# Kernel optimization log

Hardware: AMD Instinct MI355X
Metric: run time of the kernel (lower is better)

Reference implementation:

```python
import jax, jax.numpy as jnp
import numpy as np
from jax import lax

B, T, C = 4, 2048, 2048
H, S = 32, 64
HEAD_SIZE_DIVISOR = 8.0
LN_EPS = 1e-5


def setup_inputs() -> dict:
    key = jax.random.key(0)
    ks = jax.random.split(key, 12)
    scale = 0.02
    return {
        "hidden": jax.random.normal(ks[0], (B, T, C), jnp.float32),
        "state_kv": jnp.zeros((B, H, S, S), jnp.float32),
        "time_decay": jax.random.normal(ks[1], (H, S), jnp.float32) * 0.5,
        "time_faaaa": jax.random.normal(ks[2], (H, S), jnp.float32) * 0.5,
        "time_mix_key": jax.random.uniform(ks[3], (1, 1, C), jnp.float32),
        "time_mix_value": jax.random.uniform(ks[4], (1, 1, C), jnp.float32),
        "time_mix_receptance": jax.random.uniform(ks[5], (1, 1, C), jnp.float32),
        "time_mix_gate": jax.random.uniform(ks[6], (1, 1, C), jnp.float32),
        "key_w": jax.random.normal(ks[7], (C, C), jnp.float32) * scale,
        "value_w": jax.random.normal(ks[8], (C, C), jnp.float32) * scale,
        "receptance_w": jax.random.normal(ks[9], (C, C), jnp.float32) * scale,
        "gate_w": jax.random.normal(ks[10], (C, C), jnp.float32) * scale,
        "output_w": jax.random.normal(ks[11], (C, C), jnp.float32) * scale,
        "ln_w": jnp.ones((C,), jnp.float32),
        "ln_b": jnp.zeros((C,), jnp.float32),
    }


def _rwkv5_scan(r, k, v, w, u, state0):
    # r,k,v: [B,T,H,S]; w,u: [H,S]; state0: [B,H,S,S]
    w_ = w[None, :, :, None]  # decay broadcast over value dim
    u_ = u[None, :, :, None]  # time_first (bonus) broadcast over value dim

    def step(state, rkv):
        rt, kt, vt = rkv  # each [B,H,S]
        a = kt[:, :, :, None] * vt[:, :, None, :]      # outer product [B,H,S,S]
        o = jnp.einsum("bhs,bhsd->bhd", rt, u_ * a + state)
        state = a + w_ * state
        return state, o

    rt = jnp.moveaxis(r, 1, 0)  # [T,B,H,S]
    kt = jnp.moveaxis(k, 1, 0)
    vt = jnp.moveaxis(v, 1, 0)
    state_f, out = lax.scan(step, state0, (rt, kt, vt))
    return jnp.moveaxis(out, 0, 1), state_f  # [B,T,H,S], [B,H,S,S]


def reference(hidden, state_kv, time_decay, time_faaaa, time_mix_key,
              time_mix_value, time_mix_receptance, time_mix_gate,
              key_w, value_w, receptance_w, gate_w, output_w, ln_w, ln_b):
    B_, T_, C_ = hidden.shape
    H_, S_ = time_faaaa.shape

    # time shift: prepend zero row, drop last (state=None path)
    shifted = jnp.pad(hidden, ((0, 0), (1, 0), (0, 0)))[:, :-1]

    mix = lambda m: hidden * m + shifted * (1.0 - m)
    k = mix(time_mix_key) @ key_w.T
    v = mix(time_mix_value) @ value_w.T
    r = mix(time_mix_receptance) @ receptance_w.T
    gate = jax.nn.silu(mix(time_mix_gate) @ gate_w.T)

    r = r.reshape(B_, T_, H_, S_)
    k = k.reshape(B_, T_, H_, S_)
    v = v.reshape(B_, T_, H_, S_)

    w = jnp.exp(-jnp.exp(time_decay))  # [H,S]
    out, state_f = _rwkv5_scan(r, k, v, w, time_faaaa, state_kv)

    # GroupNorm over H groups of size S, applied per (b,t) row
    x = out.reshape(B_ * T_, H_, S_) / HEAD_SIZE_DIVISOR
    mu = jnp.mean(x, axis=-1, keepdims=True)
    var = jnp.var(x, axis=-1, keepdims=True)
    xn = (x - mu) * lax.rsqrt(var + LN_EPS)
    xn = xn.reshape(B_ * T_, H_ * S_) * ln_w + ln_b

    out = xn.reshape(B_, T_, C_) * gate
    out = out @ output_w.T
    return out, state_f
```

## Files before the change

### kernel.cpp

```cpp
#include <hip/hip_runtime.h>
#include <hip/hip_bf16.h>

typedef unsigned short u16;
typedef __bf16 bf16x8 __attribute__((ext_vector_type(8)));
typedef unsigned short ushort8v __attribute__((ext_vector_type(8)));
typedef float f32x4 __attribute__((ext_vector_type(4)));
typedef float f32x8 __attribute__((ext_vector_type(8)));

#define B_ 4
#define T_ 2048
#define C_ 2048
#define H_ 32
#define S_ 64

__device__ __forceinline__ u16 f2bf(float x) {
  unsigned int u = __float_as_uint(x);
  unsigned int r = (u + 0x7fffu + ((u >> 16) & 1u)) >> 16;
  return (u16)r;
}
__device__ __forceinline__ float bf2f(u16 x) {
  return __uint_as_float(((unsigned int)x) << 16);
}
__device__ __forceinline__ void gload_lds16(const void* g, void* l) {
  __builtin_amdgcn_global_load_lds(
      (const __attribute__((address_space(1))) void*)g,
      (__attribute__((address_space(3))) void*)l, 16, 0, 0);
}

#define VM10 asm volatile("s_waitcnt vmcnt(10)" ::: "memory")
#define VM8 asm volatile("s_waitcnt vmcnt(8)" ::: "memory")
#define VM0 asm volatile("s_waitcnt vmcnt(0)" ::: "memory")
#define LGKM0 asm volatile("s_waitcnt lgkmcnt(0)" ::: "memory")
#define BARR __builtin_amdgcn_s_barrier()
#define SCB __builtin_amdgcn_sched_barrier(0)

__global__ __launch_bounds__(256) void mix_cast_kernel(
    const float* __restrict__ hidden, const float* __restrict__ mixp,
    u16* __restrict__ out) {
  int idx = blockIdx.x * 256 + threadIdx.x;
  int c4 = idx & 511;
  int bt = idx >> 9;
  int t = bt & (T_ - 1);
  float4 h = reinterpret_cast<const float4*>(hidden)[idx];
  float4 m = reinterpret_cast<const float4*>(mixp)[c4];
  float4 sh = make_float4(0.f, 0.f, 0.f, 0.f);
  if (t != 0) sh = reinterpret_cast<const float4*>(hidden)[idx - 512];
  ushort4 o;
  o.x = f2bf(h.x * m.x + sh.x * (1.f - m.x));
  o.y = f2bf(h.y * m.y + sh.y * (1.f - m.y));
  o.z = f2bf(h.z * m.z + sh.z * (1.f - m.z));
  o.w = f2bf(h.w * m.w + sh.w * (1.f - m.w));
  reinterpret_cast<ushort4*>(out)[idx] = o;
}

__global__ __launch_bounds__(256) void mix4_cast_kernel(
    const float* __restrict__ hidden,
    const float* __restrict__ mK, const float* __restrict__ mV,
    const float* __restrict__ mR, const float* __restrict__ mG,
    u16* __restrict__ oK, u16* __restrict__ oV,
    u16* __restrict__ oR, u16* __restrict__ oG) {
  int idx = blockIdx.x * 256 + threadIdx.x;
  int c4 = idx & 511;
  int bt = idx >> 9;
  int t = bt & (T_ - 1);
  float4 h = reinterpret_cast<const float4*>(hidden)[idx];
  float4 sh = make_float4(0.f, 0.f, 0.f, 0.f);
  if (t != 0) sh = reinterpret_cast<const float4*>(hidden)[idx - 512];
  float4 m;
  ushort4 o;
#define DOMIX(MP, OP)                                          \
  m = reinterpret_cast<const float4*>(MP)[c4];                 \
  o.x = f2bf(h.x * m.x + sh.x * (1.f - m.x));                  \
  o.y = f2bf(h.y * m.y + sh.y * (1.f - m.y));                  \
  o.z = f2bf(h.z * m.z + sh.z * (1.f - m.z));                  \
  o.w = f2bf(h.w * m.w + sh.w * (1.f - m.w));                  \
  reinterpret_cast<ushort4*>(OP)[idx] = o;
  DOMIX(mK, oK)
  DOMIX(mV, oV)
  DOMIX(mR, oR)
  DOMIX(mG, oG)
#undef DOMIX
}

__global__ __launch_bounds__(256) void conv_bf16_kernel(
    const float* __restrict__ in, u16* __restrict__ out, int n4) {
  int i = blockIdx.x * 256 + threadIdx.x;
  if (i >= n4) return;
  float4 v = reinterpret_cast<const float4*>(in)[i];
  ushort4 o;
  o.x = f2bf(v.x); o.y = f2bf(v.y); o.z = f2bf(v.z); o.w = f2bf(v.w);
  reinterpret_cast<ushort4*>(out)[i] = o;
}

__global__ __launch_bounds__(256) void conv4_bf16_kernel(
    const float* __restrict__ w0, const float* __restrict__ w1,
    const float* __restrict__ w2, const float* __restrict__ w3,
    u16* __restrict__ o0, u16* __restrict__ o1,
    u16* __restrict__ o2, u16* __restrict__ o3) {
  int wsel = blockIdx.x >> 12;
  int i = (blockIdx.x & 4095) * 256 + threadIdx.x;
  const float* in = (wsel == 0) ? w0 : (wsel == 1) ? w1 : (wsel == 2) ? w2 : w3;
  u16* out = (wsel == 0) ? o0 : (wsel == 1) ? o1 : (wsel == 2) ? o2 : o3;
  float4 v = reinterpret_cast<const float4*>(in)[i];
  ushort4 o;
  o.x = f2bf(v.x); o.y = f2bf(v.y); o.z = f2bf(v.z); o.w = f2bf(v.w);
  reinterpret_cast<ushort4*>(out)[i] = o;
}

template <typename OT>
__global__ __launch_bounds__(512, 2) void gemm_bt256(
    const u16* __restrict__ A, const u16* __restrict__ Bm,
    OT* __restrict__ C, int M, int N, int K) {
  __shared__ u16 Asl[4][8192];
  __shared__ u16 Bsl[4][8192];
  const int tid = threadIdx.x, lane = tid & 63, w = tid >> 6;
  const int wr = w >> 2, wc = w & 3;
  const int a15 = lane & 15, g4 = lane >> 4;
  const int nbn = N >> 8;
  const int nwg = gridDim.x, bid = blockIdx.x, cpx = nwg >> 3;
  const int swz = (bid & 7) * cpx + (bid >> 3);
  const int bm = swz / nbn, bn = swz % nbn;
  const int Ar0 = bm * 256, Br0 = bn * 256;

  const int rowoff = w * 32 + (lane >> 2);
  const int colswz = ((lane & 3) ^ ((lane >> 3) & 3)) * 8;
  const u16* Agl = A + (size_t)(Ar0 + rowoff) * K + colswz;
  const u16* Bgl = Bm + (size_t)(Br0 + rowoff) * K + colswz;
  const int lb = w * 1024;

  const int rdc = (((lane >> 4) ^ ((lane >> 1) & 3))) * 8;
  const int arow = wr * 128 + a15;
  const int brow = wc * 64 + a15;

  f32x4 acc[8][4];
#pragma unroll
  for (int m = 0; m < 8; m++)
#pragma unroll
    for (int n = 0; n < 4; n++) acc[m][n] = (f32x4){0.f, 0.f, 0.f, 0.f};

  auto STA = [&](int ktile, int kk, int slot) {
    const u16* g = Agl + ktile * 64 + kk * 32;
    gload_lds16(g, &Asl[slot][lb]);
    gload_lds16(g + (size_t)16 * K, &Asl[slot][lb + 512]);
  };
  auto STB = [&](int ktile, int kk, int slot) {
    const u16* g = Bgl + ktile * 64 + kk * 32;
    gload_lds16(g, &Bsl[slot][lb]);
    gload_lds16(g + (size_t)16 * K, &Bsl[slot][lb + 512]);
  };
  auto LOADF = [&](int P, int kk, bf16x8 (&af)[8], bf16x8 (&bv)[4]) {
    const u16* As_ = Asl[P * 2 + kk];
    const u16* Bs_ = Bsl[P * 2 + kk];
#pragma unroll
    for (int mf = 0; mf < 8; mf++)
      af[mf] = __builtin_bit_cast(
          bf16x8, *reinterpret_cast<const ushort8v*>(&As_[(arow + mf * 16) * 32 + rdc]));
#pragma unroll
    for (int nf = 0; nf < 4; nf++)
      bv[nf] = __builtin_bit_cast(
          bf16x8, *reinterpret_cast<const ushort8v*>(&Bs_[(brow + nf * 16) * 32 + rdc]));
  };
  auto MM = [&](bf16x8 (&af)[8], bf16x8 (&bv)[4]) {
    __builtin_amdgcn_s_setprio(1);
#pragma unroll
    for (int mf = 0; mf < 8; mf++)
#pragma unroll
      for (int nf = 0; nf < 4; nf++)
        acc[mf][nf] =
            __builtin_amdgcn_mfma_f32_16x16x32_bf16(af[mf], bv[nf], acc[mf][nf], 0, 0, 0);
    __builtin_amdgcn_s_setprio(0);
  };

  bf16x8 f0A[8], f1A[8];
  bf16x8 f0B[4], f1B[4];

  const int NT = K >> 6;
  STA(0, 0, 0); STB(0, 0, 0);
  STA(0, 1, 1); STB(0, 1, 1);
  STA(1, 0, 2); STB(1, 0, 2);
  VM8;
  BARR;
  LOADF(0, 0, f0A, f0B);

  for (int T = 0; T + 2 < NT; ++T) {
    int P = T & 1, Q = P ^ 1;
    STA(T + 1, 1, Q * 2 + 1); STB(T + 1, 1, Q * 2 + 1);
    VM10; BARR; SCB;
    LOADF(P, 1, f1A, f1B);
    MM(f0A, f0B);
    BARR;
    STA(T + 2, 0, P * 2 + 0); STB(T + 2, 0, P * 2 + 0);
    VM10; BARR; SCB;
    LOADF(Q, 0, f0A, f0B);
    MM(f1A, f1B);
    BARR;
  }
  {
    int T = NT - 2, P = T & 1, Q = P ^ 1;
    STA(T + 1, 1, Q * 2 + 1); STB(T + 1, 1, Q * 2 + 1);
    VM10; BARR; SCB;
    LOADF(P, 1, f1A, f1B);
    MM(f0A, f0B);
    BARR;
    VM8; BARR; SCB;
    LOADF(Q, 0, f0A, f0B);
    MM(f1A, f1B);
    BARR;
  }
  {
    int P = (NT - 1) & 1;
    VM0; BARR; SCB;
    LOADF(P, 1, f1A, f1B);
    MM(f0A, f0B);
    LGKM0;
    BARR;
    MM(f1A, f1B);
  }

  if constexpr (sizeof(OT) == 2) {
    u16* ep = (w < 4) ? Asl[w] : Bsl[w - 4];
#pragma unroll
    for (int mfg = 0; mfg < 8; mfg++)
#pragma unroll
      for (int q = 0; q < 4; q++)
#pragma unroll
        for (int nf = 0; nf < 4; nf++)
          ep[(mfg * 16 + g4 * 4 + q) * 64 + nf * 16 + a15] = f2bf(acc[mfg][nf][q]);
    OT* cbase = C + (size_t)(Ar0 + wr * 128) * N + Br0 + wc * 64;
#pragma unroll
    for (int i = 0; i < 16; i++) {
      int id = lane + 64 * i;
      int row = id >> 3, k16 = id & 7;
      ushort8v v8 = *reinterpret_cast<const ushort8v*>(&ep[row * 64 + k16 * 8]);
      *reinterpret_cast<ushort8v*>(cbase + (size_t)row * N + k16 * 8) = v8;
    }
  } else {
    int crow0 = Ar0 + wr * 128 + g4 * 4;
    int ccol0 = Br0 + wc * 64 + a15;
#pragma unroll
    for (int mfg = 0; mfg < 8; mfg++) {
#pragma unroll
      for (int q = 0; q < 4; q++) {
        OT* cp = C + (size_t)(crow0 + mfg * 16 + q) * N + ccol0;
#pragma unroll
        for (int nf = 0; nf < 4; nf++) cp[nf * 16] = (OT)acc[mfg][nf][q];
      }
    }
  }
}

template <int CHL>
__global__ __launch_bounds__(64) void scan_phase1_mfma(
    const u16* __restrict__ Kb, const u16* __restrict__ Vb,
    const float* __restrict__ td, float* __restrict__ chunks) {
  constexpr int NCH = T_ / CHL;
  constexpr int LDW = CHL + 8;
  __shared__ u16 Ash[64 * LDW];
  __shared__ u16 Vsh[64 * LDW];
  int lane = threadIdx.x & 63;
  int gw = blockIdx.x;
  int c = gw & (NCH - 1), bh = gw / NCH;
  int h = bh & 31, b = bh >> 5;

  size_t base = ((size_t)b * T_ + (size_t)c * CHL) * C_ + h * 64 + lane;
  const u16* Kp = Kb + base;
  const u16* Vp = Vb + base;

  {
    float w = __expf(-__expf(td[h * 64 + lane]));
    u16* Arow = &Ash[lane * LDW];
    float p = 1.f;
#pragma unroll
    for (int i4 = CHL - 4; i4 >= 0; i4 -= 4) {
      float a3 = bf2f(Kp[(size_t)(i4 + 3) * C_]) * p; p *= w;
      float a2 = bf2f(Kp[(size_t)(i4 + 2) * C_]) * p; p *= w;
      float a1 = bf2f(Kp[(size_t)(i4 + 1) * C_]) * p; p *= w;
      float a0 = bf2f(Kp[(size_t)(i4 + 0) * C_]) * p; p *= w;
      ushort4 pk;
      pk.x = f2bf(a0); pk.y = f2bf(a1); pk.z = f2bf(a2); pk.w = f2bf(a3);
      *reinterpret_cast<ushort4*>(&Arow[i4]) = pk;
    }
  }
  {
    u16* Vrow = &Vsh[lane * LDW];
#pragma unroll
    for (int i4 = 0; i4 < CHL; i4 += 4) {
      ushort4 pk;
      pk.x = Vp[(size_t)(i4 + 0) * C_];
      pk.y = Vp[(size_t)(i4 + 1) * C_];
      pk.z = Vp[(size_t)(i4 + 2) * C_];
      pk.w = Vp[(size_t)(i4 + 3) * C_];
      *reinterpret_cast<ushort4*>(&Vrow[i4]) = pk;
    }
  }

  f32x4 acc[4][4];
#pragma unroll
  for (int m = 0; m < 4; m++)
#pragma unroll
    for (int n = 0; n < 4; n++) acc[m][n] = (f32x4){0.f, 0.f, 0.f, 0.f};

#pragma unroll
  for (int kb = 0; kb < CHL / 32; kb++) {
    int ko = kb * 32 + (lane >> 4) * 8;
    bf16x8 Af[4], Bf[4];
#pragma unroll
    for (int m = 0; m < 4; m++) {
      ushort8v t8 = *reinterpret_cast<const ushort8v*>(&Ash[(m * 16 + (lane & 15)) * LDW + ko]);
      Af[m] = __builtin_bit_cast(bf16x8, t8);
    }
#pragma unroll
    for (int n = 0; n < 4; n++) {
      ushort8v t8 = *reinterpret_cast<const ushort8v*>(&Vsh[(n * 16 + (lane & 15)) * LDW + ko]);
      Bf[n] = __builtin_bit_cast(bf16x8, t8);
    }
#pragma unroll
    for (int m = 0; m < 4; m++)
#pragma unroll
      for (int n = 0; n < 4; n++)
        acc[m][n] = __builtin_amdgcn_mfma_f32_16x16x32_bf16(Af[m], Bf[n], acc[m][n], 0, 0, 0);
  }

  float* outp = chunks + (((size_t)c * B_ + b) * H_ + h) * 4096;
  int r0 = (lane >> 4) * 4, c0 = lane & 15;
#pragma unroll
  for (int m = 0; m < 4; m++)
#pragma unroll
    for (int n = 0; n < 4; n++)
#pragma unroll
      for (int q = 0; q < 4; q++)
        outp[(size_t)(m * 16 + r0 + q) * 64 + n * 16 + c0] = acc[m][n][q];
}

template <int NCH, int CHL>
__global__ __launch_bounds__(256) void scan_phase1(
    const u16* __restrict__ Kb, const u16* __restrict__ Vb,
    const float* __restrict__ td, float* __restrict__ chunks) {
  int lane = threadIdx.x & 63;
  int gw = (blockIdx.x * 256 + threadIdx.x) >> 6;
  int c = gw & (NCH - 1), bh = gw / NCH;
  int h = bh & 31, b = bh >> 5;
  const float* tdh = td + h * 64;
  float wreg[64];
#pragma unroll
  for (int s = 0; s < 64; s++) wreg[s] = __expf(-__expf(tdh[s]));
  float st[64];
#pragma unroll
  for (int s = 0; s < 64; s++) st[s] = 0.f;
  size_t base = ((size_t)b * T_ + (size_t)c * CHL) * C_ + h * 64 + lane;
  const u16* Kp = Kb + base;
  const u16* Vp = Vb + base;
  for (int t = 0; t < CHL; t++) {
    float kcur = bf2f(Kp[(size_t)t * C_]), vcur = bf2f(Vp[(size_t)t * C_]);
#pragma unroll
    for (int s = 0; s < 64; s++) {
      float ks = __shfl(kcur, s);
      st[s] = fmaf(wreg[s], st[s], ks * vcur);
    }
  }
  float* outp = chunks + (((size_t)c * B_ + b) * H_ + h) * 4096 + lane;
#pragma unroll
  for (int s = 0; s < 64; s++) outp[s * 64] = st[s];
}

template <int NCH, int CHL>
__global__ __launch_bounds__(256) void scan_phase2(
    const float* __restrict__ st0, const float* __restrict__ td,
    float* __restrict__ chunks, float* __restrict__ state_out) {
  int idx = blockIdx.x * 256 + threadIdx.x;
  int h = (idx >> 12) & 31;
  int s = (idx >> 6) & 63;
  float wL = __expf(-(float)CHL * __expf(td[h * 64 + s]));
  float st = st0[idx];
#pragma unroll
  for (int cc = 0; cc < NCH; cc++) {
    size_t off = (size_t)cc * 524288 + idx;
    float sc = chunks[off];
    chunks[off] = st;
    st = fmaf(wL, st, sc);
  }
  state_out[idx] = st;
}

__global__ __launch_bounds__(256) void scan_phase3_mfma(
    const u16* __restrict__ Rb, const u16* __restrict__ Kb,
    const u16* __restrict__ Vb, const float* __restrict__ td,
    const float* __restrict__ tf, const float* __restrict__ chunks,
    const u16* __restrict__ Gb, const float* __restrict__ lnw,
    const float* __restrict__ lnb, u16* __restrict__ Y) {
  __shared__ __align__(16) u16 smem[4][5248];
  int lane = threadIdx.x & 63, wib = threadIdx.x >> 6;
  int gw = blockIdx.x * 4 + wib;
  int c = gw & 31, bh = gw >> 5;
  int h = bh & 31, b = bh >> 5;
  int a = lane & 15, g = lane >> 4;
  int h0 = h * 64;

  u16* Kt = smem[wib];
  u16* Vt = Kt + 1024;
  u16* StT = Vt + 1024;
  u16* AT = StT + 2560;

  f32x8 sA[2], sB[2], sC[2];
#pragma unroll
  for (int kk = 0; kk < 2; kk++) {
#pragma unroll
    for (int e = 0; e < 8; e++) {
      int s = kk * 32 + g * 8 + e;
      float ew = __expf(td[h0 + s]);
      sA[kk][e] = __expf(-(float)a * ew);
      sB[kk][e] = __expf(-((float)a - 8.f) * ew);
      sC[kk][e] = __expf(-(7.f - (float)a) * ew);
    }
  }
  f32x4 sE[4];
  f32x4 ewD;
#pragma unroll
  for (int ms = 0; ms < 4; ms++) {
    ewD[ms] = __expf(td[h0 + ms * 16 + a]);
#pragma unroll
    for (int q = 0; q < 4; q++)
      sE[ms][q] = __expf(-16.f * __expf(td[h0 + ms * 16 + g * 4 + q]));
  }

  f32x4 St[4][4];
  const float* cpc = chunks + (((size_t)c * B_ + b) * H_ + h) * 4096;
#pragma unroll
  for (int ms = 0; ms < 4; ms++)
#pragma unroll
    for (int nd = 0; nd < 4; nd++)
#pragma unroll
      for (int q = 0; q < 4; q++)
        St[ms][nd][q] = cpc[(size_t)(ms * 16 + g * 4 + q) * 64 + nd * 16 + a];

#pragma unroll
  for (int z = 0; z < 6; z++) {
    int idx = z * 64 + lane;
    int row = idx / 24, col = 16 + idx % 24;
    AT[row * 40 + col] = 0;
  }

  size_t tbase = ((size_t)b * T_ + (size_t)c * 64) * C_ + h0;

  for (int sb = 0; sb < 4; sb++) {
    size_t rb0 = tbase + (size_t)(sb * 16) * C_;

    ushort8v r8[2], k8[2];
#pragma unroll
    for (int kk = 0; kk < 2; kk++) {
      r8[kk] = *reinterpret_cast<const ushort8v*>(Rb + rb0 + (size_t)a * C_ + kk * 32 + g * 8);
      k8[kk] = *reinterpret_cast<const ushort8v*>(Kb + rb0 + (size_t)a * C_ + kk * 32 + g * 8);
    }
    {
      int srow = lane >> 3;
      int scol = (lane & 7) * 8;
      *reinterpret_cast<ushort8v*>(&Kt[srow * 64 + scol]) =
          *reinterpret_cast<const ushort8v*>(Kb + rb0 + (size_t)srow * C_ + scol);
      *reinterpret_cast<ushort8v*>(&Kt[(srow + 8) * 64 + scol]) =
          *reinterpret_cast<const ushort8v*>(Kb + rb0 + (size_t)(srow + 8) * C_ + scol);
      *reinterpret_cast<ushort8v*>(&Vt[srow * 64 + scol]) =
          *reinterpret_cast<const ushort8v*>(Vb + rb0 + (size_t)srow * C_ + scol);
      *reinterpret_cast<ushort8v*>(&Vt[(srow + 8) * 64 + scol]) =
          *reinterpret_cast<const ushort8v*>(Vb + rb0 + (size_t)(srow + 8) * C_ + scol);
    }

    f32x4 O[4];
#pragma unroll
    for (int nd = 0; nd < 4; nd++) O[nd] = (f32x4){0.f, 0.f, 0.f, 0.f};

#pragma unroll
    for (int kk = 0; kk < 2; kk++) {
#pragma unroll
      for (int msl = 0; msl < 2; msl++) {
        int ms = kk * 2 + msl;
#pragma unroll
        for (int nd = 0; nd < 4; nd++) {
          ushort4 pk;
          pk.x = f2bf(St[ms][nd][0]); pk.y = f2bf(St[ms][nd][1]);
          pk.z = f2bf(St[ms][nd][2]); pk.w = f2bf(St[ms][nd][3]);
          *reinterpret_cast<ushort4*>(&StT[(a + nd * 16) * 40 + msl * 16 + g * 4]) = pk;
        }
      }
      ushort8v rt;
#pragma unroll
      for (int e = 0; e < 8; e++) rt[e] = f2bf(bf2f(r8[kk][e]) * sA[kk][e]);
      bf16x8 rtf = __builtin_bit_cast(bf16x8, rt);
#pragma unroll
      for (int nd = 0; nd < 4; nd++) {
        ushort8v sfr = *reinterpret_cast<const ushort8v*>(&StT[(a + nd * 16) * 40 + g * 8]);
        O[nd] = __builtin_amdgcn_mfma_f32_16x16x32_bf16(
            rtf, __builtin_bit_cast(bf16x8, sfr), O[nd], 0, 0, 0);
      }
    }

    float p = 0.f;
    {
      uintptr_t ta = (uintptr_t)(tf + h0);
      asm volatile("" : "+v"(ta));
      const float* tfp = (const float*)ta;
#pragma unroll
      for (int kk = 0; kk < 2; kk++) {
        float4 t0 = *reinterpret_cast<const float4*>(tfp + kk * 32 + g * 8);
        float4 t1 = *reinterpret_cast<const float4*>(tfp + kk * 32 + g * 8 + 4);
        float tv[8] = {t0.x, t0.y, t0.z, t0.w, t1.x, t1.y, t1.z, t1.w};
#pragma unroll
        for (int e = 0; e < 8; e++)
          p = fmaf(bf2f(r8[kk][e]) * tv[e], bf2f(k8[kk][e]), p);
      }
    }
    p += __shfl_xor(p, 16);
    p += __shfl_xor(p, 32);

    f32x4 Am = (f32x4){0.f, 0.f, 0.f, 0.f};
#pragma unroll
    for (int kk = 0; kk < 2; kk++) {
      ushort8v kh, rh;
#pragma unroll
      for (int e = 0; e < 8; e++) {
        kh[e] = f2bf(bf2f(k8[kk][e]) * sC[kk][e]);
        rh[e] = f2bf(bf2f(r8[kk][e]) * sB[kk][e]);
      }
      Am = __builtin_amdgcn_mfma_f32_16x16x32_bf16(
          __builtin_bit_cast(bf16x8, kh), __builtin_bit_cast(bf16x8, rh), Am, 0, 0, 0);
    }
    {
      ushort4 aw;
#pragma unroll
      for (int q = 0; q < 4; q++) {
        int jr = g * 4 + q;
        float v = (jr < a) ? Am[q] : ((jr == a) ? p : 0.f);
        ((u16*)&aw)[q] = f2bf(v);
      }
      *reinterpret_cast<ushort4*>(&AT[a * 40 + g * 4]) = aw;
    }
    bf16x8 afrag;
    {
      ushort8v t8 = *reinterpret_cast<const ushort8v*>(&AT[a * 40 + g * 8]);
      afrag = __builtin_bit_cast(bf16x8, t8);
    }

    bf16x8 vfrag[4];
#pragma unroll
    for (int nd = 0; nd < 4; nd++) {
      ushort8v t8;
      if (g < 2) {
#pragma unroll
        for (int e = 0; e < 8; e++) t8[e] = Vt[(g * 8 + e) * 64 + a + nd * 16];
      } else {
#pragma unroll
        for (int e = 0; e < 8; e++) t8[e] = 0;
      }
      vfrag[nd] = __builtin_bit_cast(bf16x8, t8);
    }

#pragma unroll
    for (int nd = 0; nd < 4; nd++)
      O[nd] = __builtin_amdgcn_mfma_f32_16x16x32_bf16(afrag, vfrag[nd], O[nd], 0, 0, 0);

#pragma unroll
    for (int ms = 0; ms < 4; ms++)
#pragma unroll
      for (int nd = 0; nd < 4; nd++)
#pragma unroll
        for (int q = 0; q < 4; q++) St[ms][nd][q] *= sE[ms][q];

#pragma unroll
    for (int ms = 0; ms < 4; ms++) {
      ushort8v kt8;
      if (g < 2) {
#pragma unroll
        for (int e = 0; e < 8; e++) {
          int j = g * 8 + e;
          float f = bf2f(Kt[j * 64 + ms * 16 + a]) * __expf(-(15.f - (float)j) * ewD[ms]);
          kt8[e] = f2bf(f);
        }
      } else {
#pragma unroll
        for (int e = 0; e < 8; e++) kt8[e] = 0;
      }
      bf16x8 kf = __builtin_bit_cast(bf16x8, kt8);
#pragma unroll
      for (int nd = 0; nd < 4; nd++)
        St[ms][nd] = __builtin_amdgcn_mfma_f32_16x16x32_bf16(kf, vfrag[nd], St[ms][nd], 0, 0, 0);
    }

#pragma unroll
    for (int nd = 0; nd < 4; nd++)
#pragma unroll
      for (int q = 0; q < 4; q++) O[nd][q] *= 0.125f;
    {
      uintptr_t la = (uintptr_t)(lnw + h0);
      uintptr_t lba = (uintptr_t)(lnb + h0);
      asm volatile("" : "+v"(la), "+v"(lba));
      const float* lwp = (const float*)la;
      const float* lbp = (const float*)lba;
#pragma unroll
      for (int q = 0; q < 4; q++) {
        float ssum = O[0][q] + O[1][q] + O[2][q] + O[3][q];
        ssum += __shfl_xor(ssum, 1); ssum += __shfl_xor(ssum, 2);
        ssum += __shfl_xor(ssum, 4); ssum += __shfl_xor(ssum, 8);
        float mean = ssum * (1.f / 64.f);
        float vv = 0.f;
#pragma unroll
        for (int nd = 0; nd < 4; nd++) {
          float d = O[nd][q] - mean;
          vv = fmaf(d, d, vv);
        }
        vv += __shfl_xor(vv, 1); vv += __shfl_xor(vv, 2);
        vv += __shfl_xor(vv, 4); vv += __shfl_xor(vv, 8);
        float rs = rsqrtf(vv * (1.f / 64.f) + 1e-5f);
        size_t rowoff = rb0 + (size_t)(g * 4 + q) * C_;
#pragma unroll
        for (int nd = 0; nd < 4; nd++) {
          float xn = (O[nd][q] - mean) * rs;
          float gv = bf2f(Gb[rowoff + nd * 16 + a]);
          float sg = gv / (1.f + __expf(-gv));
          Y[rowoff + nd * 16 + a] = f2bf((xn * lwp[nd * 16 + a] + lbp[nd * 16 + a]) * sg);
        }
      }
    }
  }
}

template <int NCH, int CHL>
__global__ __launch_bounds__(256) void scan_phase3(
    const u16* __restrict__ Rb, const u16* __restrict__ Kb,
    const u16* __restrict__ Vb, const float* __restrict__ td,
    const float* __restrict__ tf, const float* __restrict__ chunks,
    const u16* __restrict__ Gb, const float* __restrict__ lnw,
    const float* __restrict__ lnb, u16* __restrict__ Y) {
  int lane = threadIdx.x & 63;
  int gw = (blockIdx.x * 256 + threadIdx.x) >> 6;
  int c = gw & (NCH - 1), bh = gw / NCH;
  int h = bh & 31, b = bh >> 5;
  const float* tdh = td + h * 64;
  float wreg[64];
#pragma unroll
  for (int s = 0; s < 64; s++) wreg[s] = __expf(-__expf(tdh[s]));
  float u_own = tf[h * 64 + lane];
  float lw = lnw[h * 64 + lane];
  float lb = lnb[h * 64 + lane];
  float st[64];
  const float* cp = chunks + (((size_t)c * B_ + b) * H_ + h) * 4096 + lane;
#pragma unroll
  for (int s = 0; s < 64; s++) st[s] = cp[s * 64];
  size_t base = ((size_t)b * T_ + (size_t)c * CHL) * C_ + h * 64 + lane;
  const u16* Rp = Rb + base;
  const u16* Kp = Kb + base;
  const u16* Vp = Vb + base;
  const u16* Gp = Gb + base;
  u16* Yp = Y + base;
  for (int t = 0; t < CHL; t++) {
    float rcur = bf2f(Rp[(size_t)t * C_]);
    float kcur = bf2f(Kp[(size_t)t * C_]);
    float vcur = bf2f(Vp[(size_t)t * C_]);
    float p = rcur * u_own * kcur;
#pragma unroll
    for (int off = 32; off >= 1; off >>= 1) p += __shfl_xor(p, off);
    float acc = 0.f;
#pragma unroll
    for (int s = 0; s < 64; s++) {
      float rs = __shfl(rcur, s);
      float ks = __shfl(kcur, s);
      acc = fmaf(rs, st[s], acc);
      st[s] = fmaf(wreg[s], st[s], ks * vcur);
    }
    float o = fmaf(p, vcur, acc);
    float x = o * 0.125f;
    float sum = x;
#pragma unroll
    for (int off = 32; off >= 1; off >>= 1) sum += __shfl_xor(sum, off);
    float mean = sum * (1.f / 64.f);
    float d = x - mean;
    float v2 = d * d;
#pragma unroll
    for (int off = 32; off >= 1; off >>= 1) v2 += __shfl_xor(v2, off);
    float var = v2 * (1.f / 64.f);
    float xn = d * rsqrtf(var + 1e-5f);
    float gg = bf2f(Gp[(size_t)t * C_]);
    float sg = gg / (1.f + __expf(-gg));
    Yp[(size_t)t * C_] = f2bf((xn * lw + lb) * sg);
  }
}

extern "C" void kernel_launch(void* const* d_in, const int* in_sizes, int n_in,
                              void* d_out, int out_size, void* d_ws, size_t ws_size,
                              hipStream_t stream) {
  const float* hidden = (const float*)d_in[0];
  const float* state0 = (const float*)d_in[1];
  const float* td = (const float*)d_in[2];
  const float* tf = (const float*)d_in[3];
  const float* mk = (const float*)d_in[4];
  const float* mv = (const float*)d_in[5];
  const float* mr = (const float*)d_in[6];
  const float* mg = (const float*)d_in[7];
  const float* kw = (const float*)d_in[8];
  const float* vw = (const float*)d_in[9];
  const float* rw = (const float*)d_in[10];
  const float* gw = (const float*)d_in[11];
  const float* ow = (const float*)d_in[12];
  const float* lnw = (const float*)d_in[13];
  const float* lnb = (const float*)d_in[14];

  float* out = (float*)d_out;
  float* state_f = out + (size_t)B_ * T_ * C_;

  const size_t MBe = (size_t)B_ * T_ * C_;
  const size_t chunks32 = (size_t)32 * B_ * H_ * S_ * S_ * 4;

  size_t bigNeed = 4 * MBe * 2 + (size_t)C_ * C_ * 2 + 4 * MBe * 2 + chunks32;
  bool useBig = (ws_size >= bigNeed);

  dim3 blk(256);
  int mixGrid = (B_ * T_ * C_ / 4) / 256;
  int convN4 = C_ * C_ / 4;
  int convGrid = convN4 / 256;
  int gemmGrid = (B_ * T_ / 256) * (C_ / 256);
  dim3 gblk(512);

  if (useBig) {
    char* ws = (char*)d_ws;
    u16* mixR = (u16*)ws;  ws += MBe * 2;
    u16* mixK = (u16*)ws;  ws += MBe * 2;
    u16* mixV = (u16*)ws;  ws += MBe * 2;
    u16* mixG = (u16*)ws;  ws += MBe * 2;
    u16* wb = (u16*)ws;    ws += (size_t)C_ * C_ * 2;
    u16* rb = (u16*)ws;    ws += MBe * 2;
    u16* kb = (u16*)ws;    ws += MBe * 2;
    u16* vb = (u16*)ws;    ws += MBe * 2;
    u16* gb = (u16*)ws;    ws += MBe * 2;
    float* chunks = (float*)ws;
    u16* wbK = (u16*)chunks;
    u16* wbV = wbK + (size_t)C_ * C_;
    u16* wbG = wbV + (size_t)C_ * C_;

    mix4_cast_kernel<<<mixGrid, blk, 0, stream>>>(hidden, mk, mv, mr, mg,
                                                  mixK, mixV, mixR, mixG);
    conv4_bf16_kernel<<<4 * convGrid, blk, 0, stream>>>(rw, kw, vw, gw,
                                                        wb, wbK, wbV, wbG);
    gemm_bt256<u16><<<gemmGrid, gblk, 0, stream>>>(mixR, wb, rb, B_ * T_, C_, C_);
    gemm_bt256<u16><<<gemmGrid, gblk, 0, stream>>>(mixK, wbK, kb, B_ * T_, C_, C_);
    gemm_bt256<u16><<<gemmGrid, gblk, 0, stream>>>(mixV, wbV, vb, B_ * T_, C_, C_);
    gemm_bt256<u16><<<gemmGrid, gblk, 0, stream>>>(mixG, wbG, gb, B_ * T_, C_, C_);

    scan_phase1_mfma<64><<<B_ * H_ * 32, dim3(64), 0, stream>>>(kb, vb, td, chunks);
    scan_phase2<32, 64><<<2048, blk, 0, stream>>>(state0, td, chunks, state_f);
    scan_phase3_mfma<<<(B_ * H_ * 32) / 4, blk, 0, stream>>>(rb, kb, vb, td, tf, chunks, gb, lnw, lnb, mixR);

    conv_bf16_kernel<<<convGrid, blk, 0, stream>>>(ow, wb, convN4);
    gemm_bt256<float><<<gemmGrid, gblk, 0, stream>>>(mixR, wb, out, B_ * T_, C_, C_);
    return;
  }

  char* ws = (char*)d_ws;
  u16* mixA = (u16*)ws;    ws += MBe * 2;
  u16* wb = (u16*)ws;      ws += (size_t)C_ * C_ * 2;
  u16* rb = (u16*)ws;      ws += MBe * 2;
  u16* kb = (u16*)ws;      ws += MBe * 2;
  u16* vb = (u16*)ws;      ws += MBe * 2;
  u16* gb = (u16*)ws;      ws += MBe * 2;
  float* chunks = (float*)ws;
  size_t fixed = (size_t)(ws - (char*)d_ws);
  bool use32 = (ws_size >= fixed + chunks32);

  mix_cast_kernel<<<mixGrid, blk, 0, stream>>>(hidden, mr, mixA);
  conv_bf16_kernel<<<convGrid, blk, 0, stream>>>(rw, wb, convN4);
  gemm_bt256<u16><<<gemmGrid, gblk, 0, stream>>>(mixA, wb, rb, B_ * T_, C_, C_);
  mix_cast_kernel<<<mixGrid, blk, 0, stream>>>(hidden, mk, mixA);
  conv_bf16_kernel<<<convGrid, blk, 0, stream>>>(kw, wb, convN4);
  gemm_bt256<u16><<<gemmGrid, gblk, 0, stream>>>(mixA, wb, kb, B_ * T_, C_, C_);
  mix_cast_kernel<<<mixGrid, blk, 0, stream>>>(hidden, mv, mixA);
  conv_bf16_kernel<<<convGrid, blk, 0, stream>>>(vw, wb, convN4);
  gemm_bt256<u16><<<gemmGrid, gblk, 0, stream>>>(mixA, wb, vb, B_ * T_, C_, C_);
  mix_cast_kernel<<<mixGrid, blk, 0, stream>>>(hidden, mg, mixA);
  conv_bf16_kernel<<<convGrid, blk, 0, stream>>>(gw, wb, convN4);
  gemm_bt256<u16><<<gemmGrid, gblk, 0, stream>>>(mixA, wb, gb, B_ * T_, C_, C_);

  if (use32) {
    scan_phase1_mfma<64><<<B_ * H_ * 32, dim3(64), 0, stream>>>(kb, vb, td, chunks);
    scan_phase2<32, 64><<<2048, blk, 0, stream>>>(state0, td, chunks, state_f);
    scan_phase3_mfma<<<(B_ * H_ * 32) / 4, blk, 0, stream>>>(rb, kb, vb, td, tf, chunks, gb, lnw, lnb, mixA);
  } else {
    scan_phase1<16, 128><<<(B_ * H_ * 16) / 4, blk, 0, stream>>>(kb, vb, td, chunks);
    scan_phase2<16, 128><<<2048, blk, 0, stream>>>(state0, td, chunks, state_f);
    scan_phase3<16, 128><<<(B_ * H_ * 16) / 4, blk, 0, stream>>>(rb, kb, vb, td, tf, chunks, gb, lnw, lnb, mixA);
  }

  conv_bf16_kernel<<<convGrid, blk, 0, stream>>>(ow, wb, convN4);
  gemm_bt256<float><<<gemmGrid, gblk, 0, stream>>>(mixA, wb, out, B_ * T_, C_, C_);
}
```

Measured before the change: 690.1 us.

## Split scan phase3 value dimension across two waves per chunk with shared GroupNorm stats

The chunked scan output kernel now assigns two waves to each (batch, head, chunk) unit, each owning half of the value columns. This halves per-wave state registers and MFMA work and doubles the number of waves. GroupNorm statistics become a single-pass sum and sum-of-squares, exchanged between the paired waves through shared memory with a block barrier every subblock. Each wave still redundantly loads K/V/R and builds the intra-chunk attention matrix. The one-pass variance is less numerically robust than the previous two-pass form.

```diff
diff --git a/kernel.cpp b/kernel.cpp
--- a/kernel.cpp
+++ b/kernel.cpp
@@ -382,15 +382,17 @@
   state_out[idx] = st;
 }
 
-__global__ __launch_bounds__(256) void scan_phase3_mfma(
+__global__ __launch_bounds__(256) void scan_phase3_mfma2(
     const u16* __restrict__ Rb, const u16* __restrict__ Kb,
     const u16* __restrict__ Vb, const float* __restrict__ td,
     const float* __restrict__ tf, const float* __restrict__ chunks,
     const u16* __restrict__ Gb, const float* __restrict__ lnw,
     const float* __restrict__ lnb, u16* __restrict__ Y) {
-  __shared__ __align__(16) u16 smem[4][5248];
+  __shared__ __align__(16) u16 smem[4][4096];
+  __shared__ float gnscr[2][2][2][4][4][2];
   int lane = threadIdx.x & 63, wib = threadIdx.x >> 6;
-  int gw = blockIdx.x * 4 + wib;
+  int unit = wib >> 1, wiu = wib & 1;
+  int gw = blockIdx.x * 2 + unit;
   int c = gw & 31, bh = gw >> 5;
   int h = bh & 31, b = bh >> 5;
   int a = lane & 15, g = lane >> 4;
@@ -399,9 +401,9 @@
   u16* Kt = smem[wib];
   u16* Vt = Kt + 1024;
   u16* StT = Vt + 1024;
-  u16* AT = StT + 2560;
-
-  f32x8 sA[2], sB[2], sC[2];
+  u16* AT = StT + 1280;
+
+  f32x8 sA[2], sB[2], sC[2], uA[2];
 #pragma unroll
   for (int kk = 0; kk < 2; kk++) {
 #pragma unroll
@@ -411,6 +413,7 @@
       sA[kk][e] = __expf(-(float)a * ew);
       sB[kk][e] = __expf(-((float)a - 8.f) * ew);
       sC[kk][e] = __expf(-(7.f - (float)a) * ew);
+      uA[kk][e] = tf[h0 + s];
     }
   }
   f32x4 sE[4];
@@ -422,16 +425,23 @@
     for (int q = 0; q < 4; q++)
       sE[ms][q] = __expf(-16.f * __expf(td[h0 + ms * 16 + g * 4 + q]));
   }
-
-  f32x4 St[4][4];
+  float lwv[2], lbv[2];
+#pragma unroll
+  for (int ndl = 0; ndl < 2; ndl++) {
+    int nd_g = wiu * 2 + ndl;
+    lwv[ndl] = lnw[h0 + nd_g * 16 + a];
+    lbv[ndl] = lnb[h0 + nd_g * 16 + a];
+  }
+
+  f32x4 St[4][2];
   const float* cpc = chunks + (((size_t)c * B_ + b) * H_ + h) * 4096;
 #pragma unroll
   for (int ms = 0; ms < 4; ms++)
 #pragma unroll
-    for (int nd = 0; nd < 4; nd++)
+    for (int ndl = 0; ndl < 2; ndl++)
 #pragma unroll
       for (int q = 0; q < 4; q++)
-        St[ms][nd][q] = cpc[(size_t)(ms * 16 + g * 4 + q) * 64 + nd * 16 + a];
+        St[ms][ndl][q] = cpc[(size_t)(ms * 16 + g * 4 + q) * 64 + (wiu * 2 + ndl) * 16 + a];
 
 #pragma unroll
   for (int z = 0; z < 6; z++) {
@@ -464,9 +474,9 @@
           *reinterpret_cast<const ushort8v*>(Vb + rb0 + (size_t)(srow + 8) * C_ + scol);
     }
 
-    f32x4 O[4];
-#pragma unroll
-    for (int nd = 0; nd < 4; nd++) O[nd] = (f32x4){0.f, 0.f, 0.f, 0.f};
+    f32x4 O[2];
+#pragma unroll
+    for (int ndl = 0; ndl < 2; ndl++) O[ndl] = (f32x4){0.f, 0.f, 0.f, 0.f};
 
 #pragma unroll
     for (int kk = 0; kk < 2; kk++) {
@@ -474,11 +484,11 @@
       for (int msl = 0; msl < 2; msl++) {
         int ms = kk * 2 + msl;
 #pragma unroll
-        for (int nd = 0; nd < 4; nd++) {
+        for (int ndl = 0; ndl < 2; ndl++) {
           ushort4 pk;
-          pk.x = f2bf(St[ms][nd][0]); pk.y = f2bf(St[ms][nd][1]);
-          pk.z = f2bf(St[ms][nd][2]); pk.w = f2bf(St[ms][nd][3]);
-          *reinterpret_cast<ushort4*>(&StT[(a + nd * 16) * 40 + msl * 16 + g * 4]) = pk;
+          pk.x = f2bf(St[ms][ndl][0]); pk.y = f2bf(St[ms][ndl][1]);
+          pk.z = f2bf(St[ms][ndl][2]); pk.w = f2bf(St[ms][ndl][3]);
+          *reinterpret_cast<ushort4*>(&StT[(a + ndl * 16) * 40 + msl * 16 + g * 4]) = pk;
         }
       }
       ushort8v rt;
@@ -486,28 +496,19 @@
       for (int e = 0; e < 8; e++) rt[e] = f2bf(bf2f(r8[kk][e]) * sA[kk][e]);
       bf16x8 rtf = __builtin_bit_cast(bf16x8, rt);
 #pragma unroll
-      for (int nd = 0; nd < 4; nd++) {
-        ushort8v sfr = *reinterpret_cast<const ushort8v*>(&StT[(a + nd * 16) * 40 + g * 8]);
-        O[nd] = __builtin_amdgcn_mfma_f32_16x16x32_bf16(
-            rtf, __builtin_bit_cast(bf16x8, sfr), O[nd], 0, 0, 0);
+      for (int ndl = 0; ndl < 2; ndl++) {
+        ushort8v sfr = *reinterpret_cast<const ushort8v*>(&StT[(a + ndl * 16) * 40 + g * 8]);
+        O[ndl] = __builtin_amdgcn_mfma_f32_16x16x32_bf16(
+            rtf, __builtin_bit_cast(bf16x8, sfr), O[ndl], 0, 0, 0);
       }
     }
 
     float p = 0.f;
-    {
-      uintptr_t ta = (uintptr_t)(tf + h0);
-      asm volatile("" : "+v"(ta));
-      const float* tfp = (const float*)ta;
-#pragma unroll
-      for (int kk = 0; kk < 2; kk++) {
-        float4 t0 = *reinterpret_cast<const float4*>(tfp + kk * 32 + g * 8);
-        float4 t1 = *reinterpret_cast<const float4*>(tfp + kk * 32 + g * 8 + 4);
-        float tv[8] = {t0.x, t0.y, t0.z, t0.w, t1.x, t1.y, t1.z, t1.w};
-#pragma unroll
-        for (int e = 0; e < 8; e++)
-          p = fmaf(bf2f(r8[kk][e]) * tv[e], bf2f(k8[kk][e]), p);
-      }
-    }
+#pragma unroll
+    for (int kk = 0; kk < 2; kk++)
+#pragma unroll
+      for (int e = 0; e < 8; e++)
+        p = fmaf(bf2f(r8[kk][e]) * uA[kk][e], bf2f(k8[kk][e]), p);
     p += __shfl_xor(p, 16);
     p += __shfl_xor(p, 32);
 
@@ -539,30 +540,31 @@
       afrag = __builtin_bit_cast(bf16x8, t8);
     }
 
-    bf16x8 vfrag[4];
-#pragma unroll
-    for (int nd = 0; nd < 4; nd++) {
+    bf16x8 vfrag[2];
+#pragma unroll
+    for (int ndl = 0; ndl < 2; ndl++) {
+      int nd_g = wiu * 2 + ndl;
       ushort8v t8;
       if (g < 2) {
 #pragma unroll
-        for (int e = 0; e < 8; e++) t8[e] = Vt[(g * 8 + e) * 64 + a + nd * 16];
+        for (int e = 0; e < 8; e++) t8[e] = Vt[(g * 8 + e) * 64 + a + nd_g * 16];
       } else {
 #pragma unroll
         for (int e = 0; e < 8; e++) t8[e] = 0;
       }
-      vfrag[nd] = __builtin_bit_cast(bf16x8, t8);
-    }
-
-#pragma unroll
-    for (int nd = 0; nd < 4; nd++)
-      O[nd] = __builtin_amdgcn_mfma_f32_16x16x32_bf16(afrag, vfrag[nd], O[nd], 0, 0, 0);
+      vfrag[ndl] = __builtin_bit_cast(bf16x8, t8);
+    }
+
+#pragma unroll
+    for (int ndl = 0; ndl < 2; ndl++)
+      O[ndl] = __builtin_amdgcn_mfma_f32_16x16x32_bf16(afrag, vfrag[ndl], O[ndl], 0, 0, 0);
 
 #pragma unroll
     for (int ms = 0; ms < 4; ms++)
 #pragma unroll
-      for (int nd = 0; nd < 4; nd++)
-#pragma unroll
-        for (int q = 0; q < 4; q++) St[ms][nd][q] *= sE[ms][q];
+      for (int ndl = 0; ndl < 2; ndl++)
+#pragma unroll
+        for (int q = 0; q < 4; q++) St[ms][ndl][q] *= sE[ms][q];
 
 #pragma unroll
     for (int ms = 0; ms < 4; ms++) {
@@ -580,43 +582,48 @@
       }
       bf16x8 kf = __builtin_bit_cast(bf16x8, kt8);
 #pragma unroll
-      for (int nd = 0; nd < 4; nd++)
-        St[ms][nd] = __builtin_amdgcn_mfma_f32_16x16x32_bf16(kf, vfrag[nd], St[ms][nd], 0, 0, 0);
-    }
-
-#pragma unroll
-    for (int nd = 0; nd < 4; nd++)
-#pragma unroll
-      for (int q = 0; q < 4; q++) O[nd][q] *= 0.125f;
-    {
-      uintptr_t la = (uintptr_t)(lnw + h0);
-      uintptr_t lba = (uintptr_t)(lnb + h0);
-      asm volatile("" : "+v"(la), "+v"(lba));
-      const float* lwp = (const float*)la;
-      const float* lbp = (const float*)lba;
+      for (int ndl = 0; ndl < 2; ndl++)
+        St[ms][ndl] = __builtin_amdgcn_mfma_f32_16x16x32_bf16(kf, vfrag[ndl], St[ms][ndl], 0, 0, 0);
+    }
+
+#pragma unroll
+    for (int ndl = 0; ndl < 2; ndl++)
+#pragma unroll
+      for (int q = 0; q < 4; q++) O[ndl][q] *= 0.125f;
+    float ps[4], pq[4];
+#pragma unroll
+    for (int q = 0; q < 4; q++) {
+      float s2 = O[0][q] + O[1][q];
+      float q2 = O[0][q] * O[0][q] + O[1][q] * O[1][q];
+      s2 += __shfl_xor(s2, 1); q2 += __shfl_xor(q2, 1);
+      s2 += __shfl_xor(s2, 2); q2 += __shfl_xor(q2, 2);
+      s2 += __shfl_xor(s2, 4); q2 += __shfl_xor(q2, 4);
+      s2 += __shfl_xor(s2, 8); q2 += __shfl_xor(q2, 8);
+      ps[q] = s2; pq[q] = q2;
+    }
+    if (a == 0) {
 #pragma unroll
       for (int q = 0; q < 4; q++) {
-        float ssum = O[0][q] + O[1][q] + O[2][q] + O[3][q];
-        ssum += __shfl_xor(ssum, 1); ssum += __shfl_xor(ssum, 2);
-        ssum += __shfl_xor(ssum, 4); ssum += __shfl_xor(ssum, 8);
-        float mean = ssum * (1.f / 64.f);
-        float vv = 0.f;
-#pragma unroll
-        for (int nd = 0; nd < 4; nd++) {
-          float d = O[nd][q] - mean;
-          vv = fmaf(d, d, vv);
-        }
-        vv += __shfl_xor(vv, 1); vv += __shfl_xor(vv, 2);
-        vv += __shfl_xor(vv, 4); vv += __shfl_xor(vv, 8);
-        float rs = rsqrtf(vv * (1.f / 64.f) + 1e-5f);
-        size_t rowoff = rb0 + (size_t)(g * 4 + q) * C_;
-#pragma unroll
-        for (int nd = 0; nd < 4; nd++) {
-          float xn = (O[nd][q] - mean) * rs;
-          float gv = bf2f(Gb[rowoff + nd * 16 + a]);
-          float sg = gv / (1.f + __expf(-gv));
-          Y[rowoff + nd * 16 + a] = f2bf((xn * lwp[nd * 16 + a] + lbp[nd * 16 + a]) * sg);
-        }
+        gnscr[sb & 1][unit][wiu][g][q][0] = ps[q];
+        gnscr[sb & 1][unit][wiu][g][q][1] = pq[q];
+      }
+    }
+    __syncthreads();
+#pragma unroll
+    for (int q = 0; q < 4; q++) {
+      float ts = ps[q] + gnscr[sb & 1][unit][wiu ^ 1][g][q][0];
+      float tq = pq[q] + gnscr[sb & 1][unit][wiu ^ 1][g][q][1];
+      float mean = ts * (1.f / 64.f);
+      float var = tq * (1.f / 64.f) - mean * mean;
+      float rs = rsqrtf(var + 1e-5f);
+      size_t rowoff = rb0 + (size_t)(g * 4 + q) * C_;
+#pragma unroll
+      for (int ndl = 0; ndl < 2; ndl++) {
+        int nd_g = wiu * 2 + ndl;
+        float xn = (O[ndl][q] - mean) * rs;
+        float gv = bf2f(Gb[rowoff + nd_g * 16 + a]);
+        float sg = gv / (1.f + __expf(-gv));
+        Y[rowoff + nd_g * 16 + a] = f2bf((xn * lwv[ndl] + lbv[ndl]) * sg);
       }
     }
   }
@@ -745,7 +752,7 @@
 
     scan_phase1_mfma<64><<<B_ * H_ * 32, dim3(64), 0, stream>>>(kb, vb, td, chunks);
     scan_phase2<32, 64><<<2048, blk, 0, stream>>>(state0, td, chunks, state_f);
-    scan_phase3_mfma<<<(B_ * H_ * 32) / 4, blk, 0, stream>>>(rb, kb, vb, td, tf, chunks, gb, lnw, lnb, mixR);
+    scan_phase3_mfma2<<<(B_ * H_ * 32) / 2, blk, 0, stream>>>(rb, kb, vb, td, tf, chunks, gb, lnw, lnb, mixR);
 
     conv_bf16_kernel<<<convGrid, blk, 0, stream>>>(ow, wb, convN4);
     gemm_bt256<float><<<gemmGrid, gblk, 0, stream>>>(mixR, wb, out, B_ * T_, C_, C_);
@@ -779,7 +786,7 @@
   if (use32) {
     scan_phase1_mfma<64><<<B_ * H_ * 32, dim3(64), 0, stream>>>(kb, vb, td, chunks);
     scan_phase2<32, 64><<<2048, blk, 0, stream>>>(state0, td, chunks, state_f);
-    scan_phase3_mfma<<<(B_ * H_ * 32) / 4, blk, 0, stream>>>(rb, kb, vb, td, tf, chunks, gb, lnw, lnb, mixA);
+    scan_phase3_mfma2<<<(B_ * H_ * 32) / 2, blk, 0, stream>>>(rb, kb, vb, td, tf, chunks, gb, lnw, lnb, mixA);
   } else {
     scan_phase1<16, 128><<<(B_ * H_ * 16) / 4, blk, 0, stream>>>(kb, vb, td, chunks);
     scan_phase2<16, 128><<<2048, blk, 0, stream>>>(state0, td, chunks, state_f);
```

Measured after the change: 708.7 us. +2.7%, slower.
